# Performance work log

Hardware: AMD Instinct MI355X
Metric: run time of the kernel (lower is better)

## Reference

```python
import jax, jax.numpy as jnp
import numpy as np

INPUT_SIZE = 416.0
CONF_THRESH = 0.25
IOU_THRESH = 0.45
N = 8192


def setup_inputs() -> dict:
    key = jax.random.key(0)
    preds = jax.random.normal(key, (1, 5, N), dtype=jnp.float32)
    return {"preds": preds}


def _pairwise_iou(b):
    # b: [N,4] xyxy -> iou: [N,N], matching the torch clamp(min=0) semantics
    xx1 = jnp.maximum(b[:, None, 0], b[None, :, 0])
    yy1 = jnp.maximum(b[:, None, 1], b[None, :, 1])
    xx2 = jnp.minimum(b[:, None, 2], b[None, :, 2])
    yy2 = jnp.minimum(b[:, None, 3], b[None, :, 3])
    inter = jnp.clip(xx2 - xx1, 0.0) * jnp.clip(yy2 - yy1, 0.0)
    area = jnp.clip(b[:, 2] - b[:, 0], 0.0) * jnp.clip(b[:, 3] - b[:, 1], 0.0)  # [N]
    union = area[:, None] + area[None, :] - inter
    return jnp.where(union > 0, inter / union, 0.0)


def reference(preds):
    # decode: preds [1,5,N] rows = (cx, cy, w, h, obj)
    p = preds[0].T  # [N,5]
    cx, cy, pw, ph, obj = p[:, 0], p[:, 1], p[:, 2], p[:, 3], p[:, 4]
    x1 = cx - pw * 0.5
    y1 = cy - ph * 0.5
    x2 = cx + pw * 0.5
    y2 = cy + ph * 0.5
    boxes = jnp.stack([x1, y1, x2, y2], axis=1)  # [N,4]
    scores = obj
    classes = jnp.zeros_like(scores)

    valid = scores > CONF_THRESH  # conf filter (kept as mask; invalid boxes never kept)
    # scale to absolute coords iff all coords are normalized (max <= 1)
    scale = jnp.where(jnp.max(boxes) <= 1.0, INPUT_SIZE, 1.0)
    boxes_abs = boxes * scale

    # greedy NMS over score-descending order
    order = jnp.argsort(-scores)
    b = boxes_abs[order]          # [N,4]
    s = scores[order]             # [N]
    v = valid[order]              # [N]
    c = classes[order]            # [N]

    iou = _pairwise_iou(b)        # [N,N]

    def step(suppressed, xs):
        iou_row, v_i, i = xs
        keep_i = v_i & jnp.logical_not(suppressed[i])
        suppressed = suppressed | (keep_i & (iou_row > IOU_THRESH))
        return suppressed, keep_i

    _, keep = jax.lax.scan(
        step,
        jnp.zeros((N,), dtype=bool),
        (iou, v, jnp.arange(N)),
    )  # keep: [N] bool, in sorted order

    out = jnp.stack(
        [b[:, 0] / INPUT_SIZE, b[:, 1] / INPUT_SIZE,
         b[:, 2] / INPUT_SIZE, b[:, 3] / INPUT_SIZE, s, c],
        axis=1,
    )  # [N,6]
    # fixed-shape jit-compatible output: suppressed/filtered rows are zeroed;
    # kept rows appear in descending-score order (same order torch compacts to)
    return jnp.where(keep[:, None], out, 0.0)
```

## Files before the change

### kernel.cpp

```cpp
#include <hip/hip_runtime.h>
#include <stdint.h>

typedef unsigned long long u64;
typedef unsigned int u32;

#define NBOX 8192
#define ACMAX 1024
#define NCH 16
#define CONF 0.25f
#define IOU_T 0.45f

#define OFF_CX1    256
#define OFF_CY1    (OFF_CX1 + ACMAX * 4)
#define OFF_CX2    (OFF_CX1 + 2 * ACMAX * 4)
#define OFF_CY2    (OFF_CX1 + 3 * ACMAX * 4)
#define OFF_CSC    (OFF_CX1 + 4 * ACMAX * 4)
#define OFF_CAR    (OFF_CX1 + 5 * ACMAX * 4)
#define OFF_ROFC   (OFF_CX1 + 6 * ACMAX * 4)
#define OFF_CMASKT (OFF_CX1 + 7 * ACMAX * 4)

__device__ inline u64 readlane64(u64 v, int l) {
    u32 lo = (u32)__builtin_amdgcn_readlane((int)(u32)v, l);
    u32 hi = (u32)__builtin_amdgcn_readlane((int)(u32)(v >> 32), l);
    return ((u64)hi << 32) | (u64)lo;
}

__device__ inline u32 encf(float f) {
    u32 u = __float_as_uint(f);
    return (u & 0x80000000u) ? ~u : (u | 0x80000000u);
}

__global__ void __launch_bounds__(1024) k_sort(
        const float* __restrict__ p,
        float* __restrict__ cx1, float* __restrict__ cy1,
        float* __restrict__ cx2, float* __restrict__ cy2,
        float* __restrict__ csc, float* __restrict__ car,
        int* __restrict__ rofc, float* __restrict__ out) {
    #pragma clang fp contract(off)
    int t = threadIdx.x;
    int b = blockIdx.x;
    __shared__ u64 keys[1024];
    __shared__ u32 accs[128][36];
    __shared__ u32 accs2[8][32];
    __shared__ float redm[16];
    __shared__ float s_gmax;

    int il4 = (t & 7) * 4;
    int js  = t >> 3;
    int ibase = b * 32;

    u64 Ki[4];
    #pragma unroll
    for (int q = 0; q < 4; q++) {
        int i = ibase + il4 + q;
        u32 e = encf(p[4 * NBOX + i]);
        Ki[q] = ((u64)e << 32) | ((u64)(8191 - i) << 19) | 0x1FFFFull;
    }

    u32 acc[4] = {0u, 0u, 0u, 0u};
    float mloc = -3.4e38f;
    for (int w = 0; w < 8; w++) {
        int j = w * 1024 + t;
        float cxj = p[j], cyj = p[NBOX + j];
        float pwj = p[2 * NBOX + j], phj = p[3 * NBOX + j];
        float sj = p[4 * NBOX + j];
        float hx = pwj * 0.5f, hy = phj * 0.5f;
        float x1 = cxj - hx, y1 = cyj - hy, x2 = cxj + hx, y2 = cyj + hy;
        bool act = (sj > CONF) && (x2 > x1) && (y2 > y1);
        mloc = fmaxf(mloc, fmaxf(fmaxf(x1, y1), fmaxf(x2, y2)));
        u32 e = encf(sj);
        u32 mult = act ? 65537u : 1u;
        __syncthreads();
        keys[t] = ((u64)e << 32) | ((u64)(8191 - j) << 19) | (u64)mult;
        __syncthreads();
        int base = js * 8;
        #pragma unroll
        for (int k2 = 0; k2 < 4; k2++) {
            u64 ka = keys[base + k2 * 2];
            u64 kb = keys[base + k2 * 2 + 1];
            u32 ma = (u32)ka & 0x1FFFFu;
            u32 mb = (u32)kb & 0x1FFFFu;
            #pragma unroll
            for (int q = 0; q < 4; q++) {
                acc[q] += (ka > Ki[q]) ? ma : 0u;
                acc[q] += (kb > Ki[q]) ? mb : 0u;
            }
        }
    }
    #pragma unroll
    for (int q = 0; q < 4; q++) accs[js][il4 + q] = acc[q];
    #pragma unroll
    for (int o = 32; o > 0; o >>= 1) mloc = fmaxf(mloc, __shfl_xor(mloc, o, 64));
    if ((t & 63) == 0) redm[t >> 6] = mloc;
    __syncthreads();
    if (t < 256) {
        int il = t & 31, part = t >> 5;
        u32 s = 0;
        #pragma unroll
        for (int q = 0; q < 16; q++) s += accs[part * 16 + q][il];
        accs2[part][il] = s;
    }
    if (t == 0) {
        float g = redm[0];
        #pragma unroll
        for (int k = 1; k < 16; k++) g = fmaxf(g, redm[k]);
        s_gmax = g;
    }
    __syncthreads();
    if (t < 32) {
        u32 total = 0;
        #pragma unroll
        for (int part = 0; part < 8; part++) total += accs2[part][t];
        int r = (int)(total & 0xFFFFu);
        int cr = (int)(total >> 16);
        int i = ibase + t;
        float scale = (s_gmax <= 1.0f) ? 416.0f : 1.0f;
        float cx = p[i], cy = p[NBOX + i];
        float pw = p[2 * NBOX + i], ph = p[3 * NBOX + i];
        float s = p[4 * NBOX + i];
        float hx = pw * 0.5f, hy = ph * 0.5f;
        float x1 = cx - hx, y1 = cy - hy, x2 = cx + hx, y2 = cy + hy;
        bool a = (s > CONF) && (x2 > x1) && (y2 > y1);
        float bx1 = x1 * scale, by1 = y1 * scale;
        float bx2 = x2 * scale, by2 = y2 * scale;
        float aw = fmaxf(bx2 - bx1, 0.0f);
        float ah = fmaxf(by2 - by1, 0.0f);
        float area = aw * ah;
        bool ok = a && (cr < ACMAX);
        if (ok) {
            cx1[cr] = bx1; cy1[cr] = by1; cx2[cr] = bx2; cy2[cr] = by2;
            csc[cr] = s; car[cr] = area; rofc[cr] = r;
        } else {
            bool valid = s > CONF;
            float* o = out + (size_t)r * 6;
            o[0] = valid ? bx1 / 416.0f : 0.0f;
            o[1] = valid ? by1 / 416.0f : 0.0f;
            o[2] = valid ? bx2 / 416.0f : 0.0f;
            o[3] = valid ? by2 / 416.0f : 0.0f;
            o[4] = valid ? s : 0.0f;
            o[5] = 0.0f;
        }
    }
}

__global__ void __launch_bounds__(64) k_mask(
        const float* __restrict__ cx1, const float* __restrict__ cy1,
        const float* __restrict__ cx2, const float* __restrict__ cy2,
        const float* __restrict__ car, const float* __restrict__ csc,
        u64* __restrict__ cmaskT) {
    #pragma clang fp contract(off)
    int t = threadIdx.x;
    int i0 = blockIdx.x * 64, j0 = blockIdx.y * 64;
    u64 rv = __ballot(csc[i0 + t] > CONF);
    u64 cv = __ballot(csc[j0 + t] > CONF);
    if (rv == 0ull || cv == 0ull) return;
    __shared__ float sx1[64], sy1[64], sx2[64], sy2[64], sa[64];
    sx1[t] = cx1[i0 + t]; sy1[t] = cy1[i0 + t];
    sx2[t] = cx2[i0 + t]; sy2[t] = cy2[i0 + t];
    sa[t] = car[i0 + t];
    __syncthreads();
    int j = j0 + t;
    float xj1 = cx1[j], yj1 = cy1[j], xj2 = cx2[j], yj2 = cy2[j], aj = car[j];
    u64 w = 0;
    for (int ii = 0; ii < 64; ii++) {
        float xx1 = fmaxf(sx1[ii], xj1);
        float yy1 = fmaxf(sy1[ii], yj1);
        float xx2 = fminf(sx2[ii], xj2);
        float yy2 = fminf(sy2[ii], yj2);
        float iw = fmaxf(xx2 - xx1, 0.0f);
        float ih = fmaxf(yy2 - yy1, 0.0f);
        float inter = iw * ih;
        float uni = sa[ii] + aj - inter;
        bool sup = (uni > 0.0f) && (inter / uni > IOU_T);
        w |= ((u64)(sup ? 1u : 0u)) << ii;
    }
    cmaskT[(size_t)blockIdx.x * ACMAX + j] = w;
}

__global__ void __launch_bounds__(1024) k_final(
        const float* __restrict__ csc, const u64* __restrict__ cmaskT,
        const float* __restrict__ cx1, const float* __restrict__ cy1,
        const float* __restrict__ cx2, const float* __restrict__ cy2,
        const int* __restrict__ rofc, float* __restrict__ out) {
    int t = threadIdx.x;
    __shared__ u64 keptArr[NCH];
    int wv = t >> 6;
    float s = csc[t];
    bool valid = s > CONF;
    u64 col[NCH];
    #pragma unroll
    for (int w = 0; w < NCH; w++) col[w] = cmaskT[(size_t)w * ACMAX + t];
    bool sup = false;
    for (int c = 0; c < NCH; c++) {
        if (wv == c) {
            u64 validm = __ballot(valid);
            u64 supm = __ballot(sup);
            u64 d = col[c];
            u64 kept = 0;
            u64 cand = validm & ~supm;
            while (cand) {
                int i = __builtin_ctzll(cand);
                kept |= (1ull << i);
                u64 row = readlane64(d, i);
                u64 gt = (i < 63) ? (~0ull << (i + 1)) : 0ull;
                cand = cand & ~row & gt;
            }
            if ((t & 63) == 0) keptArr[c] = kept;
        }
        __syncthreads();
        u64 k = keptArr[c];
        if (wv > c && (col[c] & k) != 0ull) sup = true;
    }
    __syncthreads();
    if (valid) {
        bool kb = (keptArr[t >> 6] >> (t & 63)) & 1ull;
        int r = rofc[t];
        float* o = out + (size_t)r * 6;
        o[0] = kb ? cx1[t] / 416.0f : 0.0f;
        o[1] = kb ? cy1[t] / 416.0f : 0.0f;
        o[2] = kb ? cx2[t] / 416.0f : 0.0f;
        o[3] = kb ? cy2[t] / 416.0f : 0.0f;
        o[4] = kb ? s : 0.0f;
        o[5] = 0.0f;
    }
}

extern "C" void kernel_launch(void* const* d_in, const int* in_sizes, int n_in,
                              void* d_out, int out_size, void* d_ws, size_t ws_size,
                              hipStream_t stream) {
    const float* preds = (const float*)d_in[0];
    float* out = (float*)d_out;
    char* ws = (char*)d_ws;
    float* cx1 = (float*)(ws + OFF_CX1);
    float* cy1 = (float*)(ws + OFF_CY1);
    float* cx2 = (float*)(ws + OFF_CX2);
    float* cy2 = (float*)(ws + OFF_CY2);
    float* csc = (float*)(ws + OFF_CSC);
    float* car = (float*)(ws + OFF_CAR);
    int* rofc  = (int*)(ws + OFF_ROFC);
    u64* cmaskT = (u64*)(ws + OFF_CMASKT);

    hipLaunchKernelGGL(k_sort, dim3(256), dim3(1024), 0, stream,
                       preds, cx1, cy1, cx2, cy2, csc, car, rofc, out);
    hipLaunchKernelGGL(k_mask, dim3(NCH, NCH), dim3(64), 0, stream,
                       cx1, cy1, cx2, cy2, car, csc, cmaskT);
    hipLaunchKernelGGL(k_final, dim3(1), dim3(1024), 0, stream,
                       csc, cmaskT, cx1, cy1, cx2, cy2, rofc, out);
}
```

Baseline: 102.0 us.

## Fuse sort, mask and NMS into one cooperative kernel with grid syncs

New measurement: 183.0 us. 79.4% more time.

```diff
diff --git a/kernel.cpp b/kernel.cpp
--- a/kernel.cpp
+++ b/kernel.cpp
@@ -1,5 +1,8 @@
 #include <hip/hip_runtime.h>
+#include <hip/hip_cooperative_groups.h>
 #include <stdint.h>
+
+namespace cg = cooperative_groups;
 
 typedef unsigned long long u64;
 typedef unsigned int u32;
@@ -18,6 +21,13 @@
 #define OFF_CAR    (OFF_CX1 + 5 * ACMAX * 4)
 #define OFF_ROFC   (OFF_CX1 + 6 * ACMAX * 4)
 #define OFF_CMASKT (OFF_CX1 + 7 * ACMAX * 4)
+#define OFF_KEYS   (OFF_CMASKT + NCH * ACMAX * 8)
+#define OFF_BX1    (OFF_KEYS + NBOX * 8)
+#define OFF_BY1    (OFF_BX1 + NBOX * 4)
+#define OFF_BX2    (OFF_BX1 + 2 * NBOX * 4)
+#define OFF_BY2    (OFF_BX1 + 3 * NBOX * 4)
+#define OFF_BSC    (OFF_BX1 + 4 * NBOX * 4)
+#define OFF_GPART  (OFF_BX1 + 5 * NBOX * 4)
 
 __device__ inline u64 readlane64(u64 v, int l) {
     u32 lo = (u32)__builtin_amdgcn_readlane((int)(u32)v, l);
@@ -30,198 +40,207 @@
     return (u & 0x80000000u) ? ~u : (u | 0x80000000u);
 }
 
-__global__ void __launch_bounds__(1024) k_sort(
+__global__ void __launch_bounds__(1024, 4) k_fused(
         const float* __restrict__ p,
         float* __restrict__ cx1, float* __restrict__ cy1,
         float* __restrict__ cx2, float* __restrict__ cy2,
         float* __restrict__ csc, float* __restrict__ car,
-        int* __restrict__ rofc, float* __restrict__ out) {
+        int* __restrict__ rofc, float* __restrict__ out,
+        u64* __restrict__ keysG,
+        float* __restrict__ bx1G, float* __restrict__ by1G,
+        float* __restrict__ bx2G, float* __restrict__ by2G,
+        float* __restrict__ bscG, u32* __restrict__ gpart,
+        u64* __restrict__ cmaskT) {
     #pragma clang fp contract(off)
+    cg::grid_group grid = cg::this_grid();
     int t = threadIdx.x;
     int b = blockIdx.x;
-    __shared__ u64 keys[1024];
+
     __shared__ u32 accs[128][36];
     __shared__ u32 accs2[8][32];
-    __shared__ float redm[16];
-    __shared__ float s_gmax;
-
-    int il4 = (t & 7) * 4;
-    int js  = t >> 3;
-    int ibase = b * 32;
-
-    u64 Ki[4];
-    #pragma unroll
-    for (int q = 0; q < 4; q++) {
-        int i = ibase + il4 + q;
-        u32 e = encf(p[4 * NBOX + i]);
-        Ki[q] = ((u64)e << 32) | ((u64)(8191 - i) << 19) | 0x1FFFFull;
-    }
-
-    u32 acc[4] = {0u, 0u, 0u, 0u};
-    float mloc = -3.4e38f;
-    for (int w = 0; w < 8; w++) {
-        int j = w * 1024 + t;
-        float cxj = p[j], cyj = p[NBOX + j];
-        float pwj = p[2 * NBOX + j], phj = p[3 * NBOX + j];
-        float sj = p[4 * NBOX + j];
-        float hx = pwj * 0.5f, hy = phj * 0.5f;
-        float x1 = cxj - hx, y1 = cyj - hy, x2 = cxj + hx, y2 = cyj + hy;
-        bool act = (sj > CONF) && (x2 > x1) && (y2 > y1);
-        mloc = fmaxf(mloc, fmaxf(fmaxf(x1, y1), fmaxf(x2, y2)));
-        u32 e = encf(sj);
-        u32 mult = act ? 65537u : 1u;
-        __syncthreads();
-        keys[t] = ((u64)e << 32) | ((u64)(8191 - j) << 19) | (u64)mult;
-        __syncthreads();
-        int base = js * 8;
-        #pragma unroll
-        for (int k2 = 0; k2 < 4; k2++) {
-            u64 ka = keys[base + k2 * 2];
-            u64 kb = keys[base + k2 * 2 + 1];
-            u32 ma = (u32)ka & 0x1FFFFu;
-            u32 mb = (u32)kb & 0x1FFFFu;
-            #pragma unroll
-            for (int q = 0; q < 4; q++) {
-                acc[q] += (ka > Ki[q]) ? ma : 0u;
-                acc[q] += (kb > Ki[q]) ? mb : 0u;
+    __shared__ u32 redE[4];
+    __shared__ u32 mpart[16][64];
+    __shared__ u64 keptArr[NCH];
+
+    {
+        float m0 = -3.4e38f;
+        if (t < 32) {
+            int i = b * 32 + t;
+            float cx = p[i], cy = p[NBOX + i];
+            float pw = p[2 * NBOX + i], ph = p[3 * NBOX + i];
+            float s = p[4 * NBOX + i];
+            float hx = pw * 0.5f, hy = ph * 0.5f;
+            float x1 = cx - hx, y1 = cy - hy, x2 = cx + hx, y2 = cy + hy;
+            bool act = (s > CONF) && (x2 > x1) && (y2 > y1);
+            u32 e = encf(s);
+            keysG[i] = ((u64)e << 32) | ((u64)(8191 - i) << 19)
+                       | (act ? 65537ull : 1ull);
+            bx1G[i] = x1; by1G[i] = y1; bx2G[i] = x2; by2G[i] = y2;
+            bscG[i] = s;
+            m0 = fmaxf(fmaxf(x1, y1), fmaxf(x2, y2));
+        }
+        if (t < 64) {
+            #pragma unroll
+            for (int o = 32; o > 0; o >>= 1)
+                m0 = fmaxf(m0, __shfl_xor(m0, o, 64));
+            if (t == 0) gpart[b] = encf(m0);
+        }
+    }
+    grid.sync();
+
+    {
+        if (t < 256) {
+            u32 v = gpart[t];
+            #pragma unroll
+            for (int o = 32; o > 0; o >>= 1) {
+                u32 w = (u32)__shfl_xor((int)v, o, 64);
+                v = v > w ? v : w;
             }
-        }
-    }
-    #pragma unroll
-    for (int q = 0; q < 4; q++) accs[js][il4 + q] = acc[q];
-    #pragma unroll
-    for (int o = 32; o > 0; o >>= 1) mloc = fmaxf(mloc, __shfl_xor(mloc, o, 64));
-    if ((t & 63) == 0) redm[t >> 6] = mloc;
-    __syncthreads();
-    if (t < 256) {
-        int il = t & 31, part = t >> 5;
-        u32 s = 0;
-        #pragma unroll
-        for (int q = 0; q < 16; q++) s += accs[part * 16 + q][il];
-        accs2[part][il] = s;
-    }
-    if (t == 0) {
-        float g = redm[0];
-        #pragma unroll
-        for (int k = 1; k < 16; k++) g = fmaxf(g, redm[k]);
-        s_gmax = g;
-    }
-    __syncthreads();
-    if (t < 32) {
-        u32 total = 0;
-        #pragma unroll
-        for (int part = 0; part < 8; part++) total += accs2[part][t];
-        int r = (int)(total & 0xFFFFu);
-        int cr = (int)(total >> 16);
-        int i = ibase + t;
-        float scale = (s_gmax <= 1.0f) ? 416.0f : 1.0f;
-        float cx = p[i], cy = p[NBOX + i];
-        float pw = p[2 * NBOX + i], ph = p[3 * NBOX + i];
-        float s = p[4 * NBOX + i];
-        float hx = pw * 0.5f, hy = ph * 0.5f;
-        float x1 = cx - hx, y1 = cy - hy, x2 = cx + hx, y2 = cy + hy;
-        bool a = (s > CONF) && (x2 > x1) && (y2 > y1);
-        float bx1 = x1 * scale, by1 = y1 * scale;
-        float bx2 = x2 * scale, by2 = y2 * scale;
-        float aw = fmaxf(bx2 - bx1, 0.0f);
-        float ah = fmaxf(by2 - by1, 0.0f);
-        float area = aw * ah;
-        bool ok = a && (cr < ACMAX);
-        if (ok) {
-            cx1[cr] = bx1; cy1[cr] = by1; cx2[cr] = bx2; cy2[cr] = by2;
-            csc[cr] = s; car[cr] = area; rofc[cr] = r;
-        } else {
-            bool valid = s > CONF;
+            if ((t & 63) == 0) redE[t >> 6] = v;
+        }
+
+        int js = t & 127;
+        int il4 = (t >> 7) * 4;
+        int ibase = b * 32;
+        u64 Ki[4];
+        #pragma unroll
+        for (int q = 0; q < 4; q++)
+            Ki[q] = keysG[ibase + il4 + q] | 0x1FFFFull;
+        u32 acc[4] = {0u, 0u, 0u, 0u};
+        #pragma unroll 8
+        for (int k = 0; k < 64; k++) {
+            u64 kj = keysG[js + (k << 7)];
+            u32 m = (u32)kj & 0x1FFFFu;
+            acc[0] += (kj > Ki[0]) ? m : 0u;
+            acc[1] += (kj > Ki[1]) ? m : 0u;
+            acc[2] += (kj > Ki[2]) ? m : 0u;
+            acc[3] += (kj > Ki[3]) ? m : 0u;
+        }
+        #pragma unroll
+        for (int q = 0; q < 4; q++) accs[js][il4 + q] = acc[q];
+        __syncthreads();
+        if (t < 256) {
+            int il = t & 31, part = t >> 5;
+            u32 ssum = 0;
+            #pragma unroll
+            for (int q = 0; q < 16; q++) ssum += accs[part * 16 + q][il];
+            accs2[part][il] = ssum;
+        }
+        __syncthreads();
+        if (t < 32) {
+            u32 total = 0;
+            #pragma unroll
+            for (int part = 0; part < 8; part++) total += accs2[part][t];
+            int r = (int)(total & 0xFFFFu);
+            int cr = (int)(total >> 16);
+            int i = ibase + t;
+            u32 eg = redE[0];
+            eg = eg > redE[1] ? eg : redE[1];
+            eg = eg > redE[2] ? eg : redE[2];
+            eg = eg > redE[3] ? eg : redE[3];
+            float scale = (eg <= 0xBF800000u) ? 416.0f : 1.0f;
+            float x1 = bx1G[i], y1 = by1G[i], x2 = bx2G[i], y2 = by2G[i];
+            float s = bscG[i];
+            bool a = (s > CONF) && (x2 > x1) && (y2 > y1);
+            float bx1 = x1 * scale, by1 = y1 * scale;
+            float bx2 = x2 * scale, by2 = y2 * scale;
+            float aw = fmaxf(bx2 - bx1, 0.0f);
+            float ah = fmaxf(by2 - by1, 0.0f);
+            float area = aw * ah;
+            bool ok = a && (cr < ACMAX);
+            if (ok) {
+                cx1[cr] = bx1; cy1[cr] = by1; cx2[cr] = bx2; cy2[cr] = by2;
+                csc[cr] = s; car[cr] = area; rofc[cr] = r;
+            } else {
+                bool valid = s > CONF;
+                float* o = out + (size_t)r * 6;
+                o[0] = valid ? bx1 / 416.0f : 0.0f;
+                o[1] = valid ? by1 / 416.0f : 0.0f;
+                o[2] = valid ? bx2 / 416.0f : 0.0f;
+                o[3] = valid ? by2 / 416.0f : 0.0f;
+                o[4] = valid ? s : 0.0f;
+                o[5] = 0.0f;
+            }
+        }
+    }
+    grid.sync();
+
+    {
+        int bi = b >> 4, bj = b & 15;
+        int jj = t & 63;
+        int rr = t >> 6;
+        int j = bj * 64 + jj;
+        float xj1 = cx1[j], yj1 = cy1[j], xj2 = cx2[j], yj2 = cy2[j];
+        float aj = car[j];
+        int ribase = bi * 64 + rr * 4;
+        u32 nib = 0;
+        #pragma unroll
+        for (int q = 0; q < 4; q++) {
+            int ri = ribase + q;
+            float xx1 = fmaxf(cx1[ri], xj1);
+            float yy1 = fmaxf(cy1[ri], yj1);
+            float xx2 = fminf(cx2[ri], xj2);
+            float yy2 = fminf(cy2[ri], yj2);
+            float iw = fmaxf(xx2 - xx1, 0.0f);
+            float ih = fmaxf(yy2 - yy1, 0.0f);
+            float inter = iw * ih;
+            float uni = car[ri] + aj - inter;
+            bool sup = (uni > 0.0f) && (inter / uni > IOU_T);
+            nib |= (sup ? 1u : 0u) << q;
+        }
+        mpart[rr][jj] = nib;
+        __syncthreads();
+        if (t < 64) {
+            u64 w = 0;
+            #pragma unroll
+            for (int r2 = 0; r2 < 16; r2++)
+                w |= ((u64)mpart[r2][t]) << (r2 * 4);
+            cmaskT[(size_t)bi * ACMAX + bj * 64 + t] = w;
+        }
+    }
+    grid.sync();
+
+    if (b == 0) {
+        int wv = t >> 6;
+        float s = csc[t];
+        bool valid = s > CONF;
+        u64 col[NCH];
+        #pragma unroll
+        for (int w = 0; w < NCH; w++)
+            col[w] = cmaskT[(size_t)w * ACMAX + t];
+        bool sup = false;
+        for (int c = 0; c < NCH; c++) {
+            if (wv == c) {
+                u64 validm = __ballot(valid);
+                u64 supm = __ballot(sup);
+                u64 d = col[c];
+                u64 kept = 0;
+                u64 cand = validm & ~supm;
+                while (cand) {
+                    int i = __builtin_ctzll(cand);
+                    kept |= (1ull << i);
+                    u64 row = readlane64(d, i);
+                    u64 gt = (i < 63) ? (~0ull << (i + 1)) : 0ull;
+                    cand = cand & ~row & gt;
+                }
+                if ((t & 63) == 0) keptArr[c] = kept;
+            }
+            __syncthreads();
+            u64 k = keptArr[c];
+            if (wv > c && (col[c] & k) != 0ull) sup = true;
+        }
+        __syncthreads();
+        if (valid) {
+            bool kb = (keptArr[t >> 6] >> (t & 63)) & 1ull;
+            int r = rofc[t];
             float* o = out + (size_t)r * 6;
-            o[0] = valid ? bx1 / 416.0f : 0.0f;
-            o[1] = valid ? by1 / 416.0f : 0.0f;
-            o[2] = valid ? bx2 / 416.0f : 0.0f;
-            o[3] = valid ? by2 / 416.0f : 0.0f;
-            o[4] = valid ? s : 0.0f;
+            o[0] = kb ? cx1[t] / 416.0f : 0.0f;
+            o[1] = kb ? cy1[t] / 416.0f : 0.0f;
+            o[2] = kb ? cx2[t] / 416.0f : 0.0f;
+            o[3] = kb ? cy2[t] / 416.0f : 0.0f;
+            o[4] = kb ? s : 0.0f;
             o[5] = 0.0f;
         }
-    }
-}
-
-__global__ void __launch_bounds__(64) k_mask(
-        const float* __restrict__ cx1, const float* __restrict__ cy1,
-        const float* __restrict__ cx2, const float* __restrict__ cy2,
-        const float* __restrict__ car, const float* __restrict__ csc,
-        u64* __restrict__ cmaskT) {
-    #pragma clang fp contract(off)
-    int t = threadIdx.x;
-    int i0 = blockIdx.x * 64, j0 = blockIdx.y * 64;
-    u64 rv = __ballot(csc[i0 + t] > CONF);
-    u64 cv = __ballot(csc[j0 + t] > CONF);
-    if (rv == 0ull || cv == 0ull) return;
-    __shared__ float sx1[64], sy1[64], sx2[64], sy2[64], sa[64];
-    sx1[t] = cx1[i0 + t]; sy1[t] = cy1[i0 + t];
-    sx2[t] = cx2[i0 + t]; sy2[t] = cy2[i0 + t];
-    sa[t] = car[i0 + t];
-    __syncthreads();
-    int j = j0 + t;
-    float xj1 = cx1[j], yj1 = cy1[j], xj2 = cx2[j], yj2 = cy2[j], aj = car[j];
-    u64 w = 0;
-    for (int ii = 0; ii < 64; ii++) {
-        float xx1 = fmaxf(sx1[ii], xj1);
-        float yy1 = fmaxf(sy1[ii], yj1);
-        float xx2 = fminf(sx2[ii], xj2);
-        float yy2 = fminf(sy2[ii], yj2);
-        float iw = fmaxf(xx2 - xx1, 0.0f);
-        float ih = fmaxf(yy2 - yy1, 0.0f);
-        float inter = iw * ih;
-        float uni = sa[ii] + aj - inter;
-        bool sup = (uni > 0.0f) && (inter / uni > IOU_T);
-        w |= ((u64)(sup ? 1u : 0u)) << ii;
-    }
-    cmaskT[(size_t)blockIdx.x * ACMAX + j] = w;
-}
-
-__global__ void __launch_bounds__(1024) k_final(
-        const float* __restrict__ csc, const u64* __restrict__ cmaskT,
-        const float* __restrict__ cx1, const float* __restrict__ cy1,
-        const float* __restrict__ cx2, const float* __restrict__ cy2,
-        const int* __restrict__ rofc, float* __restrict__ out) {
-    int t = threadIdx.x;
-    __shared__ u64 keptArr[NCH];
-    int wv = t >> 6;
-    float s = csc[t];
-    bool valid = s > CONF;
-    u64 col[NCH];
-    #pragma unroll
-    for (int w = 0; w < NCH; w++) col[w] = cmaskT[(size_t)w * ACMAX + t];
-    bool sup = false;
-    for (int c = 0; c < NCH; c++) {
-        if (wv == c) {
-            u64 validm = __ballot(valid);
-            u64 supm = __ballot(sup);
-            u64 d = col[c];
-            u64 kept = 0;
-            u64 cand = validm & ~supm;
-            while (cand) {
-                int i = __builtin_ctzll(cand);
-                kept |= (1ull << i);
-                u64 row = readlane64(d, i);
-                u64 gt = (i < 63) ? (~0ull << (i + 1)) : 0ull;
-                cand = cand & ~row & gt;
-            }
-            if ((t & 63) == 0) keptArr[c] = kept;
-        }
-        __syncthreads();
-        u64 k = keptArr[c];
-        if (wv > c && (col[c] & k) != 0ull) sup = true;
-    }
-    __syncthreads();
-    if (valid) {
-        bool kb = (keptArr[t >> 6] >> (t & 63)) & 1ull;
-        int r = rofc[t];
-        float* o = out + (size_t)r * 6;
-        o[0] = kb ? cx1[t] / 416.0f : 0.0f;
-        o[1] = kb ? cy1[t] / 416.0f : 0.0f;
-        o[2] = kb ? cx2[t] / 416.0f : 0.0f;
-        o[3] = kb ? cy2[t] / 416.0f : 0.0f;
-        o[4] = kb ? s : 0.0f;
-        o[5] = 0.0f;
     }
 }
 
@@ -239,11 +258,26 @@
     float* car = (float*)(ws + OFF_CAR);
     int* rofc  = (int*)(ws + OFF_ROFC);
     u64* cmaskT = (u64*)(ws + OFF_CMASKT);
-
-    hipLaunchKernelGGL(k_sort, dim3(256), dim3(1024), 0, stream,
-                       preds, cx1, cy1, cx2, cy2, csc, car, rofc, out);
-    hipLaunchKernelGGL(k_mask, dim3(NCH, NCH), dim3(64), 0, stream,
-                       cx1, cy1, cx2, cy2, car, csc, cmaskT);
-    hipLaunchKernelGGL(k_final, dim3(1), dim3(1024), 0, stream,
-                       csc, cmaskT, cx1, cy1, cx2, cy2, rofc, out);
-}
+    u64* keysG = (u64*)(ws + OFF_KEYS);
+    float* bx1G = (float*)(ws + OFF_BX1);
+    float* by1G = (float*)(ws + OFF_BY1);
+    float* bx2G = (float*)(ws + OFF_BX2);
+    float* by2G = (float*)(ws + OFF_BY2);
+    float* bscG = (float*)(ws + OFF_BSC);
+    u32* gpart = (u32*)(ws + OFF_GPART);
+
+    void* args[17];
+    args[0] = (void*)&preds;
+    args[1] = (void*)&cx1;  args[2] = (void*)&cy1;
+    args[3] = (void*)&cx2;  args[4] = (void*)&cy2;
+    args[5] = (void*)&csc;  args[6] = (void*)&car;
+    args[7] = (void*)&rofc; args[8] = (void*)&out;
+    args[9] = (void*)&keysG;
+    args[10] = (void*)&bx1G; args[11] = (void*)&by1G;
+    args[12] = (void*)&bx2G; args[13] = (void*)&by2G;
+    args[14] = (void*)&bscG; args[15] = (void*)&gpart;
+    args[16] = (void*)&cmaskT;
+
+    hipLaunchCooperativeKernel((const void*)k_fused, dim3(256), dim3(1024),
+                               args, 0, stream);
+}
```

## Split box decode and key build into a prep kernel before rank counting

Applied to the files above, without the earlier changes.

New measurement: 102.9 us. No clear change (+0.9%).

```diff
diff --git a/kernel.cpp b/kernel.cpp
--- a/kernel.cpp
+++ b/kernel.cpp
@@ -18,6 +18,13 @@
 #define OFF_CAR    (OFF_CX1 + 5 * ACMAX * 4)
 #define OFF_ROFC   (OFF_CX1 + 6 * ACMAX * 4)
 #define OFF_CMASKT (OFF_CX1 + 7 * ACMAX * 4)
+#define OFF_KEYS   (OFF_CMASKT + NCH * ACMAX * 8)
+#define OFF_BX1    (OFF_KEYS + NBOX * 8)
+#define OFF_BY1    (OFF_BX1 + NBOX * 4)
+#define OFF_BX2    (OFF_BX1 + 2 * NBOX * 4)
+#define OFF_BY2    (OFF_BX1 + 3 * NBOX * 4)
+#define OFF_BSC    (OFF_BX1 + 4 * NBOX * 4)
+#define OFF_GPART  (OFF_BX1 + 5 * NBOX * 4)
 
 __device__ inline u64 readlane64(u64 v, int l) {
     u32 lo = (u32)__builtin_amdgcn_readlane((int)(u32)v, l);
@@ -30,81 +37,73 @@
     return (u & 0x80000000u) ? ~u : (u | 0x80000000u);
 }
 
-__global__ void __launch_bounds__(1024) k_sort(
-        const float* __restrict__ p,
+__global__ void __launch_bounds__(256) k_prep(
+        const float* __restrict__ p, u64* __restrict__ keysG,
+        float* __restrict__ bx1G, float* __restrict__ by1G,
+        float* __restrict__ bx2G, float* __restrict__ by2G,
+        float* __restrict__ bscG, u32* __restrict__ gpart) {
+    #pragma clang fp contract(off)
+    int t = threadIdx.x, b = blockIdx.x;
+    int i = b * 256 + t;
+    float cx = p[i], cy = p[NBOX + i];
+    float pw = p[2 * NBOX + i], ph = p[3 * NBOX + i];
+    float s = p[4 * NBOX + i];
+    float hx = pw * 0.5f, hy = ph * 0.5f;
+    float x1 = cx - hx, y1 = cy - hy, x2 = cx + hx, y2 = cy + hy;
+    bool act = (s > CONF) && (x2 > x1) && (y2 > y1);
+    keysG[i] = ((u64)encf(s) << 32) | ((u64)(8191 - i) << 19)
+               | (act ? 65537ull : 1ull);
+    bx1G[i] = x1; by1G[i] = y1; bx2G[i] = x2; by2G[i] = y2; bscG[i] = s;
+    float m0 = fmaxf(fmaxf(x1, y1), fmaxf(x2, y2));
+    #pragma unroll
+    for (int o = 32; o > 0; o >>= 1) m0 = fmaxf(m0, __shfl_xor(m0, o, 64));
+    __shared__ float wm[4];
+    if ((t & 63) == 0) wm[t >> 6] = m0;
+    __syncthreads();
+    if (t == 0)
+        gpart[b] = encf(fmaxf(fmaxf(wm[0], wm[1]), fmaxf(wm[2], wm[3])));
+}
+
+__global__ void __launch_bounds__(1024) k_rank(
+        const u64* __restrict__ keysG, const u32* __restrict__ gpart,
+        const float* __restrict__ bx1G, const float* __restrict__ by1G,
+        const float* __restrict__ bx2G, const float* __restrict__ by2G,
+        const float* __restrict__ bscG,
         float* __restrict__ cx1, float* __restrict__ cy1,
         float* __restrict__ cx2, float* __restrict__ cy2,
         float* __restrict__ csc, float* __restrict__ car,
         int* __restrict__ rofc, float* __restrict__ out) {
     #pragma clang fp contract(off)
-    int t = threadIdx.x;
-    int b = blockIdx.x;
-    __shared__ u64 keys[1024];
+    int t = threadIdx.x, b = blockIdx.x;
     __shared__ u32 accs[128][36];
     __shared__ u32 accs2[8][32];
-    __shared__ float redm[16];
-    __shared__ float s_gmax;
-
-    int il4 = (t & 7) * 4;
-    int js  = t >> 3;
+
+    int js = t & 127;
+    int il4 = (t >> 7) * 4;
     int ibase = b * 32;
-
     u64 Ki[4];
     #pragma unroll
-    for (int q = 0; q < 4; q++) {
-        int i = ibase + il4 + q;
-        u32 e = encf(p[4 * NBOX + i]);
-        Ki[q] = ((u64)e << 32) | ((u64)(8191 - i) << 19) | 0x1FFFFull;
-    }
-
+    for (int q = 0; q < 4; q++)
+        Ki[q] = keysG[ibase + il4 + q] | 0x1FFFFull;
     u32 acc[4] = {0u, 0u, 0u, 0u};
-    float mloc = -3.4e38f;
-    for (int w = 0; w < 8; w++) {
-        int j = w * 1024 + t;
-        float cxj = p[j], cyj = p[NBOX + j];
-        float pwj = p[2 * NBOX + j], phj = p[3 * NBOX + j];
-        float sj = p[4 * NBOX + j];
-        float hx = pwj * 0.5f, hy = phj * 0.5f;
-        float x1 = cxj - hx, y1 = cyj - hy, x2 = cxj + hx, y2 = cyj + hy;
-        bool act = (sj > CONF) && (x2 > x1) && (y2 > y1);
-        mloc = fmaxf(mloc, fmaxf(fmaxf(x1, y1), fmaxf(x2, y2)));
-        u32 e = encf(sj);
-        u32 mult = act ? 65537u : 1u;
-        __syncthreads();
-        keys[t] = ((u64)e << 32) | ((u64)(8191 - j) << 19) | (u64)mult;
-        __syncthreads();
-        int base = js * 8;
-        #pragma unroll
-        for (int k2 = 0; k2 < 4; k2++) {
-            u64 ka = keys[base + k2 * 2];
-            u64 kb = keys[base + k2 * 2 + 1];
-            u32 ma = (u32)ka & 0x1FFFFu;
-            u32 mb = (u32)kb & 0x1FFFFu;
-            #pragma unroll
-            for (int q = 0; q < 4; q++) {
-                acc[q] += (ka > Ki[q]) ? ma : 0u;
-                acc[q] += (kb > Ki[q]) ? mb : 0u;
-            }
-        }
+    #pragma unroll 8
+    for (int k = 0; k < 64; k++) {
+        u64 kj = keysG[js + (k << 7)];
+        u32 m = (u32)kj & 0x1FFFFu;
+        acc[0] += (kj > Ki[0]) ? m : 0u;
+        acc[1] += (kj > Ki[1]) ? m : 0u;
+        acc[2] += (kj > Ki[2]) ? m : 0u;
+        acc[3] += (kj > Ki[3]) ? m : 0u;
     }
     #pragma unroll
     for (int q = 0; q < 4; q++) accs[js][il4 + q] = acc[q];
-    #pragma unroll
-    for (int o = 32; o > 0; o >>= 1) mloc = fmaxf(mloc, __shfl_xor(mloc, o, 64));
-    if ((t & 63) == 0) redm[t >> 6] = mloc;
     __syncthreads();
     if (t < 256) {
         int il = t & 31, part = t >> 5;
-        u32 s = 0;
+        u32 ssum = 0;
         #pragma unroll
-        for (int q = 0; q < 16; q++) s += accs[part * 16 + q][il];
-        accs2[part][il] = s;
-    }
-    if (t == 0) {
-        float g = redm[0];
-        #pragma unroll
-        for (int k = 1; k < 16; k++) g = fmaxf(g, redm[k]);
-        s_gmax = g;
+        for (int q = 0; q < 16; q++) ssum += accs[part * 16 + q][il];
+        accs2[part][il] = ssum;
     }
     __syncthreads();
     if (t < 32) {
@@ -114,12 +113,15 @@
         int r = (int)(total & 0xFFFFu);
         int cr = (int)(total >> 16);
         int i = ibase + t;
-        float scale = (s_gmax <= 1.0f) ? 416.0f : 1.0f;
-        float cx = p[i], cy = p[NBOX + i];
-        float pw = p[2 * NBOX + i], ph = p[3 * NBOX + i];
-        float s = p[4 * NBOX + i];
-        float hx = pw * 0.5f, hy = ph * 0.5f;
-        float x1 = cx - hx, y1 = cy - hy, x2 = cx + hx, y2 = cy + hy;
+        u32 v = gpart[t];
+        #pragma unroll
+        for (int o = 16; o > 0; o >>= 1) {
+            u32 w = (u32)__shfl_xor((int)v, o, 64);
+            v = v > w ? v : w;
+        }
+        float scale = (v <= 0xBF800000u) ? 416.0f : 1.0f;
+        float x1 = bx1G[i], y1 = by1G[i], x2 = bx2G[i], y2 = by2G[i];
+        float s = bscG[i];
         bool a = (s > CONF) && (x2 > x1) && (y2 > y1);
         float bx1 = x1 * scale, by1 = y1 * scale;
         float bx2 = x2 * scale, by2 = y2 * scale;
@@ -239,9 +241,19 @@
     float* car = (float*)(ws + OFF_CAR);
     int* rofc  = (int*)(ws + OFF_ROFC);
     u64* cmaskT = (u64*)(ws + OFF_CMASKT);
-
-    hipLaunchKernelGGL(k_sort, dim3(256), dim3(1024), 0, stream,
-                       preds, cx1, cy1, cx2, cy2, csc, car, rofc, out);
+    u64* keysG = (u64*)(ws + OFF_KEYS);
+    float* bx1G = (float*)(ws + OFF_BX1);
+    float* by1G = (float*)(ws + OFF_BY1);
+    float* bx2G = (float*)(ws + OFF_BX2);
+    float* by2G = (float*)(ws + OFF_BY2);
+    float* bscG = (float*)(ws + OFF_BSC);
+    u32* gpart = (u32*)(ws + OFF_GPART);
+
+    hipLaunchKernelGGL(k_prep, dim3(32), dim3(256), 0, stream,
+                       preds, keysG, bx1G, by1G, bx2G, by2G, bscG, gpart);
+    hipLaunchKernelGGL(k_rank, dim3(256), dim3(1024), 0, stream,
+                       keysG, gpart, bx1G, by1G, bx2G, by2G, bscG,
+                       cx1, cy1, cx2, cy2, csc, car, rofc, out);
     hipLaunchKernelGGL(k_mask, dim3(NCH, NCH), dim3(64), 0, stream,
                        cx1, cy1, cx2, cy2, car, csc, cmaskT);
     hipLaunchKernelGGL(k_final, dim3(1), dim3(1024), 0, stream,
```

## Fuse mask and final NMS kernels via atomic completion counter

Applied to the files above, without the earlier changes.

Result: slower. 108.7 us (+6.5%).

```diff
diff --git a/kernel.cpp b/kernel.cpp
--- a/kernel.cpp
+++ b/kernel.cpp
@@ -10,6 +10,7 @@
 #define CONF 0.25f
 #define IOU_T 0.45f
 
+#define OFF_DONE   0
 #define OFF_CX1    256
 #define OFF_CY1    (OFF_CX1 + ACMAX * 4)
 #define OFF_CX2    (OFF_CX1 + 2 * ACMAX * 4)
@@ -35,10 +36,12 @@
         float* __restrict__ cx1, float* __restrict__ cy1,
         float* __restrict__ cx2, float* __restrict__ cy2,
         float* __restrict__ csc, float* __restrict__ car,
-        int* __restrict__ rofc, float* __restrict__ out) {
+        int* __restrict__ rofc, float* __restrict__ out,
+        u32* __restrict__ doneCnt) {
     #pragma clang fp contract(off)
     int t = threadIdx.x;
     int b = blockIdx.x;
+    if (b == 0 && t == 0) *doneCnt = 0u;
     __shared__ u64 keys[1024];
     __shared__ u32 accs[128][36];
     __shared__ u32 accs2[8][32];
@@ -143,47 +146,57 @@
     }
 }
 
-__global__ void __launch_bounds__(64) k_mask(
+__global__ void __launch_bounds__(1024) k_maskfinal(
         const float* __restrict__ cx1, const float* __restrict__ cy1,
         const float* __restrict__ cx2, const float* __restrict__ cy2,
         const float* __restrict__ car, const float* __restrict__ csc,
-        u64* __restrict__ cmaskT) {
+        const int* __restrict__ rofc, u64* __restrict__ cmaskT,
+        u32* __restrict__ doneCnt, float* __restrict__ out) {
     #pragma clang fp contract(off)
     int t = threadIdx.x;
-    int i0 = blockIdx.x * 64, j0 = blockIdx.y * 64;
-    u64 rv = __ballot(csc[i0 + t] > CONF);
-    u64 cv = __ballot(csc[j0 + t] > CONF);
-    if (rv == 0ull || cv == 0ull) return;
-    __shared__ float sx1[64], sy1[64], sx2[64], sy2[64], sa[64];
-    sx1[t] = cx1[i0 + t]; sy1[t] = cy1[i0 + t];
-    sx2[t] = cx2[i0 + t]; sy2[t] = cy2[i0 + t];
-    sa[t] = car[i0 + t];
-    __syncthreads();
-    int j = j0 + t;
-    float xj1 = cx1[j], yj1 = cy1[j], xj2 = cx2[j], yj2 = cy2[j], aj = car[j];
-    u64 w = 0;
-    for (int ii = 0; ii < 64; ii++) {
-        float xx1 = fmaxf(sx1[ii], xj1);
-        float yy1 = fmaxf(sy1[ii], yj1);
-        float xx2 = fminf(sx2[ii], xj2);
-        float yy2 = fminf(sy2[ii], yj2);
-        float iw = fmaxf(xx2 - xx1, 0.0f);
-        float ih = fmaxf(yy2 - yy1, 0.0f);
-        float inter = iw * ih;
-        float uni = sa[ii] + aj - inter;
-        bool sup = (uni > 0.0f) && (inter / uni > IOU_T);
-        w |= ((u64)(sup ? 1u : 0u)) << ii;
-    }
-    cmaskT[(size_t)blockIdx.x * ACMAX + j] = w;
-}
-
-__global__ void __launch_bounds__(1024) k_final(
-        const float* __restrict__ csc, const u64* __restrict__ cmaskT,
-        const float* __restrict__ cx1, const float* __restrict__ cy1,
-        const float* __restrict__ cx2, const float* __restrict__ cy2,
-        const int* __restrict__ rofc, float* __restrict__ out) {
-    int t = threadIdx.x;
+    int b = blockIdx.x;
+    if (b < 16) {
+        __shared__ float sx1[64], sy1[64], sx2[64], sy2[64], sa[64];
+        if (t < 64) {
+            sx1[t] = cx1[b * 64 + t]; sy1[t] = cy1[b * 64 + t];
+            sx2[t] = cx2[b * 64 + t]; sy2[t] = cy2[b * 64 + t];
+            sa[t]  = car[b * 64 + t];
+        }
+        __syncthreads();
+        int lane = t & 63;
+        int j = t;
+        u64 rv = __ballot(csc[b * 64 + lane] > CONF);
+        u64 cv = __ballot(csc[j] > CONF);
+        if (rv != 0ull && cv != 0ull) {
+            float xj1 = cx1[j], yj1 = cy1[j];
+            float xj2 = cx2[j], yj2 = cy2[j], aj = car[j];
+            u64 w = 0;
+            for (int ii = 0; ii < 64; ii++) {
+                float xx1 = fmaxf(sx1[ii], xj1);
+                float yy1 = fmaxf(sy1[ii], yj1);
+                float xx2 = fminf(sx2[ii], xj2);
+                float yy2 = fminf(sy2[ii], yj2);
+                float iw = fmaxf(xx2 - xx1, 0.0f);
+                float ih = fmaxf(yy2 - yy1, 0.0f);
+                float inter = iw * ih;
+                float uni = sa[ii] + aj - inter;
+                bool sup = (uni > 0.0f) && (inter / uni > IOU_T);
+                w |= ((u64)(sup ? 1u : 0u)) << ii;
+            }
+            cmaskT[(size_t)b * ACMAX + j] = w;
+        }
+        __syncthreads();
+        if (t == 0)
+            __hip_atomic_fetch_add(doneCnt, 1u, __ATOMIC_RELEASE,
+                                   __HIP_MEMORY_SCOPE_AGENT);
+        return;
+    }
     __shared__ u64 keptArr[NCH];
+    if (t == 0) {
+        while (__hip_atomic_load(doneCnt, __ATOMIC_ACQUIRE,
+                                 __HIP_MEMORY_SCOPE_AGENT) < 16u) {}
+    }
+    __syncthreads();
     int wv = t >> 6;
     float s = csc[t];
     bool valid = s > CONF;
@@ -231,6 +244,7 @@
     const float* preds = (const float*)d_in[0];
     float* out = (float*)d_out;
     char* ws = (char*)d_ws;
+    u32* doneCnt = (u32*)(ws + OFF_DONE);
     float* cx1 = (float*)(ws + OFF_CX1);
     float* cy1 = (float*)(ws + OFF_CY1);
     float* cx2 = (float*)(ws + OFF_CX2);
@@ -241,9 +255,7 @@
     u64* cmaskT = (u64*)(ws + OFF_CMASKT);
 
     hipLaunchKernelGGL(k_sort, dim3(256), dim3(1024), 0, stream,
-                       preds, cx1, cy1, cx2, cy2, csc, car, rofc, out);
-    hipLaunchKernelGGL(k_mask, dim3(NCH, NCH), dim3(64), 0, stream,
-                       cx1, cy1, cx2, cy2, car, csc, cmaskT);
-    hipLaunchKernelGGL(k_final, dim3(1), dim3(1024), 0, stream,
-                       csc, cmaskT, cx1, cy1, cx2, cy2, rofc, out);
-}
+                       preds, cx1, cy1, cx2, cy2, csc, car, rofc, out, doneCnt);
+    hipLaunchKernelGGL(k_maskfinal, dim3(17), dim3(1024), 0, stream,
+                       cx1, cy1, cx2, cy2, car, csc, rofc, cmaskT, doneCnt, out);
+}
```
